# Kernel tuning notes

Measured on AMD Instinct MI355X. Metric: run time of the kernel, lower is better.

Reference implementation:

```python
import jax, jax.numpy as jnp
import numpy as np

G, NPG, C, H, F, L = 256, 128, 16, 128, 128, 3
N = G * NPG          # 32768 nodes
E = 524288           # 16 edges per node on average
REG, REG_C = 0.01, 0.01
LN_EPS = 1e-5


def setup_inputs() -> dict:
    key = jax.random.key(0)
    ks = jax.random.split(key, 20)
    x = jax.random.normal(ks[0], (N, F), dtype=jnp.float32)
    # edges kept within each graph so dense pooling matches to_dense_batch semantics
    epg = E // G
    offs = jnp.repeat(jnp.arange(G, dtype=jnp.int64) * NPG, epg)
    src = jax.random.randint(ks[1], (E,), 0, NPG, dtype=jnp.int64) + offs
    tgt = jax.random.randint(ks[2], (E,), 0, NPG, dtype=jnp.int64) + offs
    edge_index = jnp.stack([src, tgt])
    mask_breaks = jax.random.bernoulli(ks[3], 0.5, (E,))
    s = jax.random.uniform(ks[4], (N, C), dtype=jnp.float32)
    batch = jnp.repeat(jnp.arange(G, dtype=jnp.int64), NPG)
    sc = 1.0 / np.sqrt(H)
    Wn = jax.random.normal(ks[5], (L, H, H), dtype=jnp.float32) * sc
    bn_ = jax.random.normal(ks[6], (L, H), dtype=jnp.float32) * sc
    Wo = jax.random.normal(ks[7], (L, H, H), dtype=jnp.float32) * sc
    bo = jax.random.normal(ks[8], (L, H), dtype=jnp.float32) * sc
    Wr = jax.random.normal(ks[9], (L, H, H), dtype=jnp.float32) * sc
    ln_g = jnp.ones((L, H), dtype=jnp.float32)
    ln_b = jnp.zeros((L, H), dtype=jnp.float32)
    fln_g = jnp.ones((H,), dtype=jnp.float32)
    fln_b = jnp.zeros((H,), dtype=jnp.float32)
    lin_w = jax.random.normal(ks[10], (1, H), dtype=jnp.float32) * sc
    bias = jnp.zeros((1,), dtype=jnp.float32)
    return {"x": x, "edge_index": edge_index, "mask_breaks": mask_breaks, "s": s,
            "batch": batch, "Wn": Wn, "bn_": bn_, "Wo": Wo, "bo": bo, "Wr": Wr,
            "ln_g": ln_g, "ln_b": ln_b, "fln_g": fln_g, "fln_b": fln_b,
            "lin_w": lin_w, "bias": bias}


def _layernorm(h, g, b):
    mu = jnp.mean(h, axis=-1, keepdims=True)
    v = jnp.mean(jnp.square(h - mu), axis=-1, keepdims=True)
    return (h - mu) * jax.lax.rsqrt(v + LN_EPS) * g + b


def reference(x, edge_index, mask_breaks, s, batch, Wn, bn_, Wo, bo, Wr,
              ln_g, ln_b, fln_g, fln_b, lin_w, bias):
    src, tgt = edge_index[0], edge_index[1]
    ones_e = jnp.ones((E,), dtype=x.dtype)
    cnt = jax.ops.segment_sum(ones_e, tgt, num_segments=N)          # in-degree
    inv_cnt = (1.0 / jnp.maximum(cnt, 1.0))[:, None]
    h = x
    for i in range(L):
        x_in = h @ Wn[i].T + bn_[i]
        x_out = h @ Wo[i].T + bo[i]
        x_root = h @ Wr[i].T
        msg = jnp.where(mask_breaks[:, None], x_in[src], x_out[src])  # [E,H]
        agg = jax.ops.segment_sum(msg, tgt, num_segments=N) * inv_cnt  # mean aggr
        h = jax.nn.relu(_layernorm(agg + x_root, ln_g[i], ln_b[i]))
    # dense per-graph views (equal-size graphs, batch ids sorted -> reshape)
    xd = h.reshape(G, NPG, H)
    sd = s.reshape(G, NPG, C)
    pooled = jnp.einsum("gnc,gnh->gch", sd, xd)                      # [G,C,H]
    pooled = _layernorm(pooled, fln_g, fln_b)
    xc = pooled @ lin_w.T                                            # [G,C,1]
    col_sum = sd.sum(axis=1)                                          # [G,C]
    cmask = (col_sum > 0)[..., None]
    xc = xc * cmask.astype(xc.dtype)
    out = xc.sum(axis=1) + bias                                      # [G,1]
    reg_loss = jnp.abs(Wo).sum() + jnp.abs(bo).sum()
    denom = (cmask.astype(xc.dtype).squeeze(-1) + 1e-7).sum(axis=1, keepdims=True)
    l1_loss = (jnp.abs(xc).sum(axis=1) / denom).mean()
    losses = REG * reg_loss + REG_C * l1_loss
    return out, losses, xc
```

## Files before the change

### kernel.cpp

```cpp
#include <hip/hip_runtime.h>

#define NN   32768
#define HD   128
#define EE   524288
#define GG   256
#define EPG  2048
#define CCd  16
#define LLd  3

typedef short short8 __attribute__((ext_vector_type(8)));
typedef float f32x4 __attribute__((ext_vector_type(4)));

__device__ __forceinline__ unsigned short f2bf(float f) {
  unsigned u = __builtin_bit_cast(unsigned, f);
  return (unsigned short)((u + 0x7FFFu + ((u >> 16) & 1u)) >> 16);
}
__device__ __forceinline__ unsigned bfpack(float a, float b) {
  return (unsigned)f2bf(a) | ((unsigned)f2bf(b) << 16);
}

__global__ __launch_bounds__(256) void convert_w_kernel(const float* __restrict__ Wn, const float* __restrict__ Wo,
                                                        const float* __restrict__ Wr, const float* __restrict__ bo,
                                                        unsigned* __restrict__ Wnb, unsigned* __restrict__ Wob,
                                                        unsigned* __restrict__ Wrb, float* __restrict__ wsreg) {
  int i = blockIdx.x * 256 + threadIdx.x;
  float4 a = *(const float4*)(Wn + (size_t)i * 4);
  float4 b = *(const float4*)(Wo + (size_t)i * 4);
  float4 c = *(const float4*)(Wr + (size_t)i * 4);
  *(uint2*)(Wnb + (size_t)i * 2) = make_uint2(bfpack(a.x, a.y), bfpack(a.z, a.w));
  *(uint2*)(Wob + (size_t)i * 2) = make_uint2(bfpack(b.x, b.y), bfpack(b.z, b.w));
  *(uint2*)(Wrb + (size_t)i * 2) = make_uint2(bfpack(c.x, c.y), bfpack(c.z, c.w));
  float s = fabsf(b.x) + fabsf(b.y) + fabsf(b.z) + fabsf(b.w);
  if (blockIdx.x == 0 && threadIdx.x < 96) {
    float4 d = *(const float4*)(bo + threadIdx.x * 4);
    s += fabsf(d.x) + fabsf(d.y) + fabsf(d.z) + fabsf(d.w);
  }
#pragma unroll
  for (int mk = 1; mk < 64; mk <<= 1) s += __shfl_xor(s, mk, 64);
  if ((threadIdx.x & 63) == 0) atomicAdd(wsreg, s);
}

__global__ __launch_bounds__(256) void build_m_kernel(const int* __restrict__ src, const int* __restrict__ tgt,
                                                      const int* __restrict__ mask,
                                                      unsigned* __restrict__ Mb, float* __restrict__ fin,
                                                      float* __restrict__ fout) {
  __shared__ unsigned Mi[2 * 128 * 64];
  const int g = blockIdx.x;
  const int tid = threadIdx.x;
  for (int i = tid; i < 16384; i += 256) Mi[i] = 0;
  __syncthreads();
  const int e0 = g * EPG;
#pragma unroll
  for (int i = 0; i < 8; ++i) {
    int e = e0 + i * 256 + tid;
    int t = tgt[e] & 127;
    int sl = src[e] & 127;
    int dir = (mask[e] != 0) ? 0 : 1;
    atomicAdd(&Mi[dir * 8192 + t * 64 + (sl >> 1)], 1u << ((sl & 1) * 16));
  }
  __syncthreads();
  const int t = tid >> 1, p = tid & 1;
  unsigned nin = 0, nout = 0;
#pragma unroll 4
  for (int k = 0; k < 32; ++k) { unsigned v = Mi[t * 64 + p * 32 + k]; nin += (v & 0xffffu) + (v >> 16); }
#pragma unroll 4
  for (int k = 0; k < 32; ++k) { unsigned v = Mi[8192 + t * 64 + p * 32 + k]; nout += (v & 0xffffu) + (v >> 16); }
  nin += __shfl_xor((int)nin, 1);
  nout += __shfl_xor((int)nout, 1);
  unsigned dg = nin + nout;
  float inv = 1.0f / (float)(dg > 0 ? dg : 1);
  if (p == 0) { fin[g * 128 + t] = (float)nin * inv; fout[g * 128 + t] = (float)nout * inv; }
#pragma unroll
  for (int dir = 0; dir < 2; ++dir) {
    int base = dir * 8192 + t * 64 + p * 32;
#pragma unroll
    for (int k4 = 0; k4 < 8; ++k4) {
      uint4 v = *(const uint4*)&Mi[base + k4 * 4];
      uint4 o;
      o.x = bfpack((float)(v.x & 0xffffu) * inv, (float)(v.x >> 16) * inv);
      o.y = bfpack((float)(v.y & 0xffffu) * inv, (float)(v.y >> 16) * inv);
      o.z = bfpack((float)(v.z & 0xffffu) * inv, (float)(v.z >> 16) * inv);
      o.w = bfpack((float)(v.w & 0xffffu) * inv, (float)(v.w >> 16) * inv);
      *(uint4*)&Mb[(size_t)g * 16384 + base + k4 * 4] = o;
    }
  }
}

struct PF { uint4 a, b; };
__device__ __forceinline__ PF pf_load(const unsigned short* __restrict__ srcb, int tid) {
  int row = tid >> 2, c = tid & 3;
  const unsigned short* p = srcb + row * 128 + c * 8;
  PF r;
  r.a = *(const uint4*)p;
  r.b = *(const uint4*)(p + 32);
  return r;
}
__device__ __forceinline__ void pf_store(unsigned short* __restrict__ buf, const PF& r, int tid) {
  int row = tid >> 2, c = tid & 3;
  *(uint4*)(buf + row * 72 + c * 8) = r.a;
  *(uint4*)(buf + row * 72 + (c + 4) * 8) = r.b;
}
__device__ __forceinline__ const unsigned short* stage_ptr(int sIdx, const unsigned short* Mg,
                                                           const unsigned short* Wnb, const unsigned short* Wob,
                                                           const unsigned short* Wrb) {
  if (sIdx > 29) sIdx = 29;
  int L = sIdx / 10;
  int r = sIdx - L * 10;
  int half = r & 1;
  int op = r >> 1;
  const unsigned short* base;
  if (op == 0) base = Mg;
  else if (op == 1) base = Wnb + L * 16384;
  else if (op == 2) base = Mg + 16384;
  else if (op == 3) base = Wob + L * 16384;
  else base = Wrb + L * 16384;
  return base + half * 64;
}

__global__ __launch_bounds__(512) void fused_kernel(
    const float* __restrict__ x, const unsigned short* __restrict__ Mb,
    const unsigned short* __restrict__ Wnb, const unsigned short* __restrict__ Wob,
    const unsigned short* __restrict__ Wrb,
    const float* __restrict__ bn, const float* __restrict__ bo,
    const float* __restrict__ fin, const float* __restrict__ fout,
    const float* __restrict__ lng, const float* __restrict__ lnb,
    const float* __restrict__ s,
    const float* __restrict__ flng, const float* __restrict__ flnb,
    const float* __restrict__ linw, const float* __restrict__ bias,
    float* __restrict__ out, float* __restrict__ l1g) {
  __shared__ unsigned short hTs[128 * 136];
  __shared__ unsigned short sTs[16 * 136];
  __shared__ unsigned short buf[128 * 72];
  __shared__ float colsumS[CCd];
  __shared__ float xcs[CCd], axcs[CCd], msk[CCd];

  const int g = blockIdx.x;
  const int tid = threadIdx.x;
  const int wave = tid >> 6;
  const int lane = tid & 63;
  const int m = lane & 15;
  const int q = lane >> 4;
  const int t0 = wave << 4;
  const unsigned short* Mg = Mb + (size_t)g * 32768;

  int sIdx = 0;
  PF pf = pf_load(stage_ptr(0, Mg, Wnb, Wob, Wrb), tid);

  {
    const float4* xg = (const float4*)(x + (size_t)g * 16384);
#pragma unroll
    for (int i = 0; i < 8; ++i) {
      int flat = i * 512 + tid;
      int t = flat >> 5, f0 = (flat & 31) << 2;
      float4 v = xg[flat];
      hTs[(f0 + 0) * 136 + t] = f2bf(v.x);
      hTs[(f0 + 1) * 136 + t] = f2bf(v.y);
      hTs[(f0 + 2) * 136 + t] = f2bf(v.z);
      hTs[(f0 + 3) * 136 + t] = f2bf(v.w);
    }
    int t = tid >> 2, c0 = (tid & 3) << 2;
    float4 v = *(const float4*)(s + (size_t)g * 2048 + t * 16 + c0);
    sTs[(c0 + 0) * 136 + t] = f2bf(v.x);
    sTs[(c0 + 1) * 136 + t] = f2bf(v.y);
    sTs[(c0 + 2) * 136 + t] = f2bf(v.z);
    sTs[(c0 + 3) * 136 + t] = f2bf(v.w);
    if (tid < CCd) {
      float cs = 0.f;
      for (int tt = 0; tt < 128; ++tt) cs += s[(size_t)g * 2048 + tt * 16 + tid];
      colsumS[tid] = cs;
    }
  }

  for (int L = 0; L < LLd; ++L) {
    f32x4 pre[8];
#pragma unroll
    for (int ct = 0; ct < 8; ++ct) pre[ct] = (f32x4){0.f, 0.f, 0.f, 0.f};

    for (int sg = 0; sg < 2; ++sg) {
      f32x4 accT[8];
#pragma unroll
      for (int ft = 0; ft < 8; ++ft) accT[ft] = (f32x4){0.f, 0.f, 0.f, 0.f};
#pragma unroll
      for (int half = 0; half < 2; ++half) {
        __syncthreads();
        pf_store(buf, pf, tid);
        ++sIdx;
        pf = pf_load(stage_ptr(sIdx, Mg, Wnb, Wob, Wrb), tid);
        __syncthreads();
#pragma unroll
        for (int ksl = 0; ksl < 2; ++ksl) {
          const int ksg = half * 2 + ksl;
          short8 bfr = *(const short8*)&buf[(t0 + m) * 72 + ksl * 32 + q * 8];
#pragma unroll
          for (int ft = 0; ft < 8; ++ft) {
            short8 afr = *(const short8*)&hTs[(ft * 16 + m) * 136 + ksg * 32 + q * 8];
            accT[ft] = __builtin_amdgcn_mfma_f32_16x16x32_bf16(afr, bfr, accT[ft], 0, 0, 0);
          }
        }
      }
#pragma unroll
      for (int half = 0; half < 2; ++half) {
        __syncthreads();
        pf_store(buf, pf, tid);
        ++sIdx;
        pf = pf_load(stage_ptr(sIdx, Mg, Wnb, Wob, Wrb), tid);
        __syncthreads();
#pragma unroll
        for (int ksl = 0; ksl < 2; ++ksl) {
          const int ksg = half * 2 + ksl;
          f32x4 lo = accT[2 * ksg], hi = accT[2 * ksg + 1];
          short8 afr;
#pragma unroll
          for (int j = 0; j < 8; ++j) {
            int srcl = ((((q & 1) << 1) + (j >> 2)) << 4) + m;
            float ylo = __shfl(lo[j & 3], srcl, 64);
            float yhi = __shfl(hi[j & 3], srcl, 64);
            afr[j] = (short)f2bf((q >> 1) ? yhi : ylo);
          }
#pragma unroll
          for (int ct = 0; ct < 8; ++ct) {
            short8 bfr = *(const short8*)&buf[(ct * 16 + m) * 72 + ksl * 32 + q * 8];
            pre[ct] = __builtin_amdgcn_mfma_f32_16x16x32_bf16(afr, bfr, pre[ct], 0, 0, 0);
          }
        }
      }
    }
#pragma unroll
    for (int half = 0; half < 2; ++half) {
      __syncthreads();
      pf_store(buf, pf, tid);
      ++sIdx;
      pf = pf_load(stage_ptr(sIdx, Mg, Wnb, Wob, Wrb), tid);
      __syncthreads();
#pragma unroll
      for (int ksl = 0; ksl < 2; ++ksl) {
        const int ksg = half * 2 + ksl;
        short8 afr;
#pragma unroll
        for (int j = 0; j < 8; ++j)
          afr[j] = (short)hTs[(ksg * 32 + q * 8 + j) * 136 + t0 + m];
#pragma unroll
        for (int ct = 0; ct < 8; ++ct) {
          short8 bfr = *(const short8*)&buf[(ct * 16 + m) * 72 + ksl * 32 + q * 8];
          pre[ct] = __builtin_amdgcn_mfma_f32_16x16x32_bf16(afr, bfr, pre[ct], 0, 0, 0);
        }
      }
    }
    float bnv[8], bov[8], gv[8], bv[8];
#pragma unroll
    for (int ct = 0; ct < 8; ++ct) {
      int c = L * 128 + ct * 16 + m;
      bnv[ct] = bn[c]; bov[ct] = bo[c]; gv[ct] = lng[c]; bv[ct] = lnb[c];
    }
#pragma unroll
    for (int r = 0; r < 4; ++r) {
      const int tl = q * 4 + r;
      const int T = g * 128 + t0 + tl;
      const float fiv = fin[T], fov = fout[T];
      float v[8];
      float sum = 0.f;
#pragma unroll
      for (int ct = 0; ct < 8; ++ct) {
        v[ct] = pre[ct][r] + fiv * bnv[ct] + fov * bov[ct];
        sum += v[ct];
      }
      sum += __shfl_xor(sum, 1); sum += __shfl_xor(sum, 2);
      sum += __shfl_xor(sum, 4); sum += __shfl_xor(sum, 8);
      const float mu = sum * (1.0f / 128.0f);
      float sq = 0.f;
#pragma unroll
      for (int ct = 0; ct < 8; ++ct) { float d = v[ct] - mu; sq += d * d; }
      sq += __shfl_xor(sq, 1); sq += __shfl_xor(sq, 2);
      sq += __shfl_xor(sq, 4); sq += __shfl_xor(sq, 8);
      const float rstd = rsqrtf(sq * (1.0f / 128.0f) + 1e-5f);
#pragma unroll
      for (int ct = 0; ct < 8; ++ct) {
        float o = fmaxf((v[ct] - mu) * rstd * gv[ct] + bv[ct], 0.0f);
        hTs[(ct * 16 + m) * 136 + t0 + tl] = f2bf(o);
      }
    }
  }

  __syncthreads();
  f32x4 pl = (f32x4){0.f, 0.f, 0.f, 0.f};
#pragma unroll
  for (int ks = 0; ks < 4; ++ks) {
    short8 a = *(const short8*)&sTs[m * 136 + ks * 32 + q * 8];
    short8 b = *(const short8*)&hTs[(wave * 16 + m) * 136 + ks * 32 + q * 8];
    pl = __builtin_amdgcn_mfma_f32_16x16x32_bf16(a, b, pl, 0, 0, 0);
  }
  float* pooledS = (float*)buf;
#pragma unroll
  for (int r = 0; r < 4; ++r) pooledS[(q * 4 + r) * 132 + wave * 16 + m] = pl[r];
  __syncthreads();

  if (tid < 256) {
    const int c = tid >> 4;
    const int j0 = (tid & 15) << 3;
    float v[8];
#pragma unroll
    for (int jj = 0; jj < 8; ++jj) v[jj] = pooledS[c * 132 + j0 + jj];
    float sum = 0.f;
#pragma unroll
    for (int jj = 0; jj < 8; ++jj) sum += v[jj];
#pragma unroll
    for (int mk = 1; mk < 16; mk <<= 1) sum += __shfl_xor(sum, mk, 64);
    float mu = sum * (1.0f / 128.0f);
    float sq = 0.f;
#pragma unroll
    for (int jj = 0; jj < 8; ++jj) { float d = v[jj] - mu; sq += d * d; }
#pragma unroll
    for (int mk = 1; mk < 16; mk <<= 1) sq += __shfl_xor(sq, mk, 64);
    float rstd = rsqrtf(sq * (1.0f / 128.0f) + 1e-5f);
    float dot = 0.f;
#pragma unroll
    for (int jj = 0; jj < 8; ++jj) {
      float nv = (v[jj] - mu) * rstd * flng[j0 + jj] + flnb[j0 + jj];
      dot += nv * linw[j0 + jj];
    }
#pragma unroll
    for (int mk = 1; mk < 16; mk <<= 1) dot += __shfl_xor(dot, mk, 64);
    if ((tid & 15) == 0) {
      float cm = (colsumS[c] > 0.f) ? 1.0f : 0.0f;
      float xcv = dot * cm;
      out[257 + g * CCd + c] = xcv;
      xcs[c] = xcv; axcs[c] = fabsf(xcv); msk[c] = cm;
    }
  }
  __syncthreads();
  if (tid == 0) {
    float so = 0.f, sa = 0.f, sd = 0.f;
#pragma unroll
    for (int k = 0; k < CCd; ++k) { so += xcs[k]; sa += axcs[k]; sd += msk[k] + 1e-7f; }
    out[g] = so + bias[0];
    l1g[g] = sa / sd;
  }
}

__global__ __launch_bounds__(256) void combine_kernel(const float* __restrict__ l1g, const float* __restrict__ wsreg,
                                                      float* __restrict__ outp) {
  const int tid = threadIdx.x;
  float s2 = l1g[tid];
#pragma unroll
  for (int mk = 1; mk < 64; mk <<= 1) s2 += __shfl_xor(s2, mk, 64);
  __shared__ float rs2[4];
  if ((tid & 63) == 0) rs2[tid >> 6] = s2;
  __syncthreads();
  if (tid == 0) {
    float l1 = (rs2[0] + rs2[1] + rs2[2] + rs2[3]) * (1.0f / GG);
    outp[0] = 0.01f * wsreg[0] + 0.01f * l1;
  }
}

extern "C" void kernel_launch(void* const* d_in, const int* in_sizes, int n_in,
                              void* d_out, int out_size, void* d_ws, size_t ws_size,
                              hipStream_t stream) {
  (void)in_sizes; (void)n_in; (void)out_size; (void)ws_size;
  const float* x    = (const float*)d_in[0];
  const int*   ei   = (const int*)d_in[1];
  const int*   mask = (const int*)d_in[2];
  const float* s    = (const float*)d_in[3];
  const float* Wn   = (const float*)d_in[5];
  const float* bn   = (const float*)d_in[6];
  const float* Wo   = (const float*)d_in[7];
  const float* bo   = (const float*)d_in[8];
  const float* Wr   = (const float*)d_in[9];
  const float* lng  = (const float*)d_in[10];
  const float* lnb  = (const float*)d_in[11];
  const float* flng = (const float*)d_in[12];
  const float* flnb = (const float*)d_in[13];
  const float* linw = (const float*)d_in[14];
  const float* bias = (const float*)d_in[15];
  float* out = (float*)d_out;

  char* ws = (char*)d_ws;
  size_t off = 0;
  auto alloc = [&](size_t b) { char* p = ws + off; off += (b + 255) & ~(size_t)255; return p; };
  unsigned short* Mbuf = (unsigned short*)alloc((size_t)GG * 2 * 128 * 128 * 2);
  float* fin    = (float*)alloc((size_t)NN * 4);
  float* fout   = (float*)alloc((size_t)NN * 4);
  unsigned short* Wnb = (unsigned short*)alloc((size_t)LLd * HD * HD * 2);
  unsigned short* Wob = (unsigned short*)alloc((size_t)LLd * HD * HD * 2);
  unsigned short* Wrb = (unsigned short*)alloc((size_t)LLd * HD * HD * 2);
  float* l1g    = (float*)alloc((size_t)GG * 4);
  float* wsreg  = (float*)alloc(256);

  const int* srcA = ei;
  const int* tgtA = ei + EE;

  hipMemsetAsync(wsreg, 0, 4, stream);
  convert_w_kernel<<<LLd * HD * HD / (256 * 4), 256, 0, stream>>>(Wn, Wo, Wr, bo,
      (unsigned*)Wnb, (unsigned*)Wob, (unsigned*)Wrb, wsreg);
  build_m_kernel<<<GG, 256, 0, stream>>>(srcA, tgtA, mask, (unsigned*)Mbuf, fin, fout);
  fused_kernel<<<GG, 512, 0, stream>>>(x, Mbuf, Wnb, Wob, Wrb, bn, bo, fin, fout,
                                       lng, lnb, s, flng, flnb, linw, bias, out, l1g);
  combine_kernel<<<1, 256, 0, stream>>>(l1g, wsreg, out + 256);
}
```

Before: 157.3 us.

## Fuse adjacency build into main kernel and keep adjacency fragments in registers

Removes the separate build_m kernel and its global bf16 adjacency buffer. Each block now builds per-graph edge counts in shared memory, computes degrees and normalized bf16 MFMA fragments directly into registers, and stores fin/fout in shared memory. The staged shared-memory prefetch of weights is replaced by direct global (L2-cached) loads of the bf16 weight fragments, which removes many syncthreads. The x transpose is also rewritten to pack pairs of nodes per store. The costs are higher register pressure from holding the fragments plus a launch-bounds hint, and weight reads that now go through cache rather than shared memory.

```diff
diff --git a/kernel.cpp b/kernel.cpp
--- a/kernel.cpp
+++ b/kernel.cpp
@@ -40,99 +40,22 @@
   if ((threadIdx.x & 63) == 0) atomicAdd(wsreg, s);
 }
 
-__global__ __launch_bounds__(256) void build_m_kernel(const int* __restrict__ src, const int* __restrict__ tgt,
-                                                      const int* __restrict__ mask,
-                                                      unsigned* __restrict__ Mb, float* __restrict__ fin,
-                                                      float* __restrict__ fout) {
-  __shared__ unsigned Mi[2 * 128 * 64];
-  const int g = blockIdx.x;
-  const int tid = threadIdx.x;
-  for (int i = tid; i < 16384; i += 256) Mi[i] = 0;
-  __syncthreads();
-  const int e0 = g * EPG;
-#pragma unroll
-  for (int i = 0; i < 8; ++i) {
-    int e = e0 + i * 256 + tid;
-    int t = tgt[e] & 127;
-    int sl = src[e] & 127;
-    int dir = (mask[e] != 0) ? 0 : 1;
-    atomicAdd(&Mi[dir * 8192 + t * 64 + (sl >> 1)], 1u << ((sl & 1) * 16));
-  }
-  __syncthreads();
-  const int t = tid >> 1, p = tid & 1;
-  unsigned nin = 0, nout = 0;
-#pragma unroll 4
-  for (int k = 0; k < 32; ++k) { unsigned v = Mi[t * 64 + p * 32 + k]; nin += (v & 0xffffu) + (v >> 16); }
-#pragma unroll 4
-  for (int k = 0; k < 32; ++k) { unsigned v = Mi[8192 + t * 64 + p * 32 + k]; nout += (v & 0xffffu) + (v >> 16); }
-  nin += __shfl_xor((int)nin, 1);
-  nout += __shfl_xor((int)nout, 1);
-  unsigned dg = nin + nout;
-  float inv = 1.0f / (float)(dg > 0 ? dg : 1);
-  if (p == 0) { fin[g * 128 + t] = (float)nin * inv; fout[g * 128 + t] = (float)nout * inv; }
-#pragma unroll
-  for (int dir = 0; dir < 2; ++dir) {
-    int base = dir * 8192 + t * 64 + p * 32;
-#pragma unroll
-    for (int k4 = 0; k4 < 8; ++k4) {
-      uint4 v = *(const uint4*)&Mi[base + k4 * 4];
-      uint4 o;
-      o.x = bfpack((float)(v.x & 0xffffu) * inv, (float)(v.x >> 16) * inv);
-      o.y = bfpack((float)(v.y & 0xffffu) * inv, (float)(v.y >> 16) * inv);
-      o.z = bfpack((float)(v.z & 0xffffu) * inv, (float)(v.z >> 16) * inv);
-      o.w = bfpack((float)(v.w & 0xffffu) * inv, (float)(v.w >> 16) * inv);
-      *(uint4*)&Mb[(size_t)g * 16384 + base + k4 * 4] = o;
-    }
-  }
-}
-
-struct PF { uint4 a, b; };
-__device__ __forceinline__ PF pf_load(const unsigned short* __restrict__ srcb, int tid) {
-  int row = tid >> 2, c = tid & 3;
-  const unsigned short* p = srcb + row * 128 + c * 8;
-  PF r;
-  r.a = *(const uint4*)p;
-  r.b = *(const uint4*)(p + 32);
-  return r;
-}
-__device__ __forceinline__ void pf_store(unsigned short* __restrict__ buf, const PF& r, int tid) {
-  int row = tid >> 2, c = tid & 3;
-  *(uint4*)(buf + row * 72 + c * 8) = r.a;
-  *(uint4*)(buf + row * 72 + (c + 4) * 8) = r.b;
-}
-__device__ __forceinline__ const unsigned short* stage_ptr(int sIdx, const unsigned short* Mg,
-                                                           const unsigned short* Wnb, const unsigned short* Wob,
-                                                           const unsigned short* Wrb) {
-  if (sIdx > 29) sIdx = 29;
-  int L = sIdx / 10;
-  int r = sIdx - L * 10;
-  int half = r & 1;
-  int op = r >> 1;
-  const unsigned short* base;
-  if (op == 0) base = Mg;
-  else if (op == 1) base = Wnb + L * 16384;
-  else if (op == 2) base = Mg + 16384;
-  else if (op == 3) base = Wob + L * 16384;
-  else base = Wrb + L * 16384;
-  return base + half * 64;
-}
-
-__global__ __launch_bounds__(512) void fused_kernel(
-    const float* __restrict__ x, const unsigned short* __restrict__ Mb,
+__global__ __launch_bounds__(512, 2) void fused_kernel(
+    const float* __restrict__ x,
+    const int* __restrict__ esrc, const int* __restrict__ etgt, const int* __restrict__ emask,
     const unsigned short* __restrict__ Wnb, const unsigned short* __restrict__ Wob,
     const unsigned short* __restrict__ Wrb,
     const float* __restrict__ bn, const float* __restrict__ bo,
-    const float* __restrict__ fin, const float* __restrict__ fout,
     const float* __restrict__ lng, const float* __restrict__ lnb,
     const float* __restrict__ s,
     const float* __restrict__ flng, const float* __restrict__ flnb,
     const float* __restrict__ linw, const float* __restrict__ bias,
     float* __restrict__ out, float* __restrict__ l1g) {
-  __shared__ unsigned short hTs[128 * 136];
-  __shared__ unsigned short sTs[16 * 136];
-  __shared__ unsigned short buf[128 * 72];
-  __shared__ float colsumS[CCd];
-  __shared__ float xcs[CCd], axcs[CCd], msk[CCd];
+  __shared__ __align__(16) unsigned short hTs[128 * 136];
+  __shared__ __align__(16) unsigned short sTs[16 * 136];
+  __shared__ __align__(16) unsigned cnt[2 * 128 * 64];
+  __shared__ float finS[128], foutS[128];
+  __shared__ float colsumS[CCd], xcs[CCd], axcs[CCd], msk[CCd];
 
   const int g = blockIdx.x;
   const int tid = threadIdx.x;
@@ -141,34 +64,97 @@
   const int m = lane & 15;
   const int q = lane >> 4;
   const int t0 = wave << 4;
-  const unsigned short* Mg = Mb + (size_t)g * 32768;
-
-  int sIdx = 0;
-  PF pf = pf_load(stage_ptr(0, Mg, Wnb, Wob, Wrb), tid);
 
   {
-    const float4* xg = (const float4*)(x + (size_t)g * 16384);
-#pragma unroll
-    for (int i = 0; i < 8; ++i) {
-      int flat = i * 512 + tid;
-      int t = flat >> 5, f0 = (flat & 31) << 2;
-      float4 v = xg[flat];
-      hTs[(f0 + 0) * 136 + t] = f2bf(v.x);
-      hTs[(f0 + 1) * 136 + t] = f2bf(v.y);
-      hTs[(f0 + 2) * 136 + t] = f2bf(v.z);
-      hTs[(f0 + 3) * 136 + t] = f2bf(v.w);
-    }
-    int t = tid >> 2, c0 = (tid & 3) << 2;
-    float4 v = *(const float4*)(s + (size_t)g * 2048 + t * 16 + c0);
-    sTs[(c0 + 0) * 136 + t] = f2bf(v.x);
-    sTs[(c0 + 1) * 136 + t] = f2bf(v.y);
-    sTs[(c0 + 2) * 136 + t] = f2bf(v.z);
-    sTs[(c0 + 3) * 136 + t] = f2bf(v.w);
-    if (tid < CCd) {
+    uint4* cz = (uint4*)cnt;
+#pragma unroll
+    for (int i = 0; i < 8; ++i) cz[i * 512 + tid] = make_uint4(0u, 0u, 0u, 0u);
+
+    const float* xg = x + (size_t)g * 16384;
+    unsigned* hw = (unsigned*)hTs;
+#pragma unroll
+    for (int i = 0; i < 4; ++i) {
+      int task = i * 512 + tid;
+      int t2 = task & 63;
+      int f0 = (task >> 6) << 2;
+      float4 va = *(const float4*)(xg + (2 * t2) * 128 + f0);
+      float4 vb = *(const float4*)(xg + (2 * t2 + 1) * 128 + f0);
+      hw[(f0 + 0) * 68 + t2] = bfpack(va.x, vb.x);
+      hw[(f0 + 1) * 68 + t2] = bfpack(va.y, vb.y);
+      hw[(f0 + 2) * 68 + t2] = bfpack(va.z, vb.z);
+      hw[(f0 + 3) * 68 + t2] = bfpack(va.w, vb.w);
+    }
+    {
+      int t = tid >> 2, c0 = (tid & 3) << 2;
+      float4 v = *(const float4*)(s + (size_t)g * 2048 + t * 16 + c0);
+      sTs[(c0 + 0) * 136 + t] = f2bf(v.x);
+      sTs[(c0 + 1) * 136 + t] = f2bf(v.y);
+      sTs[(c0 + 2) * 136 + t] = f2bf(v.z);
+      sTs[(c0 + 3) * 136 + t] = f2bf(v.w);
+    }
+    if (tid < 64) {
+      int c = tid & 15, qq = tid >> 4;
       float cs = 0.f;
-      for (int tt = 0; tt < 128; ++tt) cs += s[(size_t)g * 2048 + tt * 16 + tid];
-      colsumS[tid] = cs;
-    }
+      for (int tt = qq; tt < 128; tt += 4) cs += s[(size_t)g * 2048 + tt * 16 + c];
+      cs += __shfl_xor(cs, 16); cs += __shfl_xor(cs, 32);
+      if (qq == 0) colsumS[c] = cs;
+    }
+  }
+  __syncthreads();
+
+  {
+    const int e0 = g * EPG;
+#pragma unroll
+    for (int i = 0; i < 4; ++i) {
+      int e = e0 + i * 512 + tid;
+      int t = etgt[e] & 127;
+      int sl = esrc[e] & 127;
+      int dir = (emask[e] != 0) ? 0 : 1;
+      atomicAdd(&cnt[dir * 8192 + t * 64 + (sl >> 1)], 1u << ((sl & 1) * 16));
+    }
+  }
+  __syncthreads();
+
+  short8 mfr[2][2][2];
+  {
+    const int t = t0 + m;
+    unsigned nin = 0, nout = 0;
+    uint4 cw[2][2][2];
+#pragma unroll
+    for (int d = 0; d < 2; ++d)
+#pragma unroll
+      for (int hf = 0; hf < 2; ++hf)
+#pragma unroll
+        for (int ksl = 0; ksl < 2; ++ksl) {
+          uint4 v = *(const uint4*)&cnt[d * 8192 + t * 64 + hf * 32 + ksl * 16 + q * 4];
+          cw[d][hf][ksl] = v;
+          unsigned ssum = (v.x & 0xffffu) + (v.x >> 16) + (v.y & 0xffffu) + (v.y >> 16)
+                        + (v.z & 0xffffu) + (v.z >> 16) + (v.w & 0xffffu) + (v.w >> 16);
+          if (d == 0) nin += ssum; else nout += ssum;
+        }
+    nin += __shfl_xor((int)nin, 16);  nin += __shfl_xor((int)nin, 32);
+    nout += __shfl_xor((int)nout, 16); nout += __shfl_xor((int)nout, 32);
+    unsigned dg = nin + nout;
+    float inv = 1.0f / (float)(dg > 0 ? dg : 1);
+    if (q == 0) { finS[t] = (float)nin * inv; foutS[t] = (float)nout * inv; }
+#pragma unroll
+    for (int d = 0; d < 2; ++d)
+#pragma unroll
+      for (int hf = 0; hf < 2; ++hf)
+#pragma unroll
+        for (int ksl = 0; ksl < 2; ++ksl) {
+          uint4 v = cw[d][hf][ksl];
+          short8 f;
+          f[0] = (short)f2bf((float)(v.x & 0xffffu) * inv);
+          f[1] = (short)f2bf((float)(v.x >> 16) * inv);
+          f[2] = (short)f2bf((float)(v.y & 0xffffu) * inv);
+          f[3] = (short)f2bf((float)(v.y >> 16) * inv);
+          f[4] = (short)f2bf((float)(v.z & 0xffffu) * inv);
+          f[5] = (short)f2bf((float)(v.z >> 16) * inv);
+          f[6] = (short)f2bf((float)(v.w & 0xffffu) * inv);
+          f[7] = (short)f2bf((float)(v.w >> 16) * inv);
+          mfr[d][hf][ksl] = f;
+        }
   }
 
   for (int L = 0; L < LLd; ++L) {
@@ -176,38 +162,29 @@
 #pragma unroll
     for (int ct = 0; ct < 8; ++ct) pre[ct] = (f32x4){0.f, 0.f, 0.f, 0.f};
 
+#pragma unroll
     for (int sg = 0; sg < 2; ++sg) {
+      const unsigned short* Wg = (sg == 0 ? Wnb : Wob) + L * 16384;
       f32x4 accT[8];
 #pragma unroll
       for (int ft = 0; ft < 8; ++ft) accT[ft] = (f32x4){0.f, 0.f, 0.f, 0.f};
 #pragma unroll
-      for (int half = 0; half < 2; ++half) {
-        __syncthreads();
-        pf_store(buf, pf, tid);
-        ++sIdx;
-        pf = pf_load(stage_ptr(sIdx, Mg, Wnb, Wob, Wrb), tid);
-        __syncthreads();
-#pragma unroll
-        for (int ksl = 0; ksl < 2; ++ksl) {
-          const int ksg = half * 2 + ksl;
-          short8 bfr = *(const short8*)&buf[(t0 + m) * 72 + ksl * 32 + q * 8];
+      for (int hf = 0; hf < 2; ++hf)
+#pragma unroll
+        for (int ksl = 0; ksl < 2; ++ksl) {
+          const int ksg = hf * 2 + ksl;
+          short8 bfr = mfr[sg][hf][ksl];
 #pragma unroll
           for (int ft = 0; ft < 8; ++ft) {
             short8 afr = *(const short8*)&hTs[(ft * 16 + m) * 136 + ksg * 32 + q * 8];
             accT[ft] = __builtin_amdgcn_mfma_f32_16x16x32_bf16(afr, bfr, accT[ft], 0, 0, 0);
           }
         }
-      }
-#pragma unroll
-      for (int half = 0; half < 2; ++half) {
-        __syncthreads();
-        pf_store(buf, pf, tid);
-        ++sIdx;
-        pf = pf_load(stage_ptr(sIdx, Mg, Wnb, Wob, Wrb), tid);
-        __syncthreads();
-#pragma unroll
-        for (int ksl = 0; ksl < 2; ++ksl) {
-          const int ksg = half * 2 + ksl;
+#pragma unroll
+      for (int hf = 0; hf < 2; ++hf)
+#pragma unroll
+        for (int ksl = 0; ksl < 2; ++ksl) {
+          const int ksg = hf * 2 + ksl;
           f32x4 lo = accT[2 * ksg], hi = accT[2 * ksg + 1];
           short8 afr;
 #pragma unroll
@@ -219,69 +196,67 @@
           }
 #pragma unroll
           for (int ct = 0; ct < 8; ++ct) {
-            short8 bfr = *(const short8*)&buf[(ct * 16 + m) * 72 + ksl * 32 + q * 8];
+            short8 bfr = *(const short8*)&Wg[(ct * 16 + m) * 128 + ksg * 32 + q * 8];
             pre[ct] = __builtin_amdgcn_mfma_f32_16x16x32_bf16(afr, bfr, pre[ct], 0, 0, 0);
           }
         }
+    }
+    {
+      const unsigned short* Wrg = Wrb + L * 16384;
+#pragma unroll
+      for (int hf = 0; hf < 2; ++hf)
+#pragma unroll
+        for (int ksl = 0; ksl < 2; ++ksl) {
+          const int ksg = hf * 2 + ksl;
+          short8 afr;
+#pragma unroll
+          for (int j = 0; j < 8; ++j)
+            afr[j] = (short)hTs[(ksg * 32 + q * 8 + j) * 136 + t0 + m];
+#pragma unroll
+          for (int ct = 0; ct < 8; ++ct) {
+            short8 bfr = *(const short8*)&Wrg[(ct * 16 + m) * 128 + ksg * 32 + q * 8];
+            pre[ct] = __builtin_amdgcn_mfma_f32_16x16x32_bf16(afr, bfr, pre[ct], 0, 0, 0);
+          }
+        }
+    }
+    __syncthreads();
+    {
+      float bnv[8], bov[8], gv[8], bv[8];
+#pragma unroll
+      for (int ct = 0; ct < 8; ++ct) {
+        int c = L * 128 + ct * 16 + m;
+        bnv[ct] = bn[c]; bov[ct] = bo[c]; gv[ct] = lng[c]; bv[ct] = lnb[c];
       }
-    }
-#pragma unroll
-    for (int half = 0; half < 2; ++half) {
-      __syncthreads();
-      pf_store(buf, pf, tid);
-      ++sIdx;
-      pf = pf_load(stage_ptr(sIdx, Mg, Wnb, Wob, Wrb), tid);
-      __syncthreads();
-#pragma unroll
-      for (int ksl = 0; ksl < 2; ++ksl) {
-        const int ksg = half * 2 + ksl;
-        short8 afr;
-#pragma unroll
-        for (int j = 0; j < 8; ++j)
-          afr[j] = (short)hTs[(ksg * 32 + q * 8 + j) * 136 + t0 + m];
+#pragma unroll
+      for (int r = 0; r < 4; ++r) {
+        const int tl = q * 4 + r;
+        const float fiv = finS[t0 + tl], fov = foutS[t0 + tl];
+        float v[8];
+        float sum = 0.f;
 #pragma unroll
         for (int ct = 0; ct < 8; ++ct) {
-          short8 bfr = *(const short8*)&buf[(ct * 16 + m) * 72 + ksl * 32 + q * 8];
-          pre[ct] = __builtin_amdgcn_mfma_f32_16x16x32_bf16(afr, bfr, pre[ct], 0, 0, 0);
+          v[ct] = pre[ct][r] + fiv * bnv[ct] + fov * bov[ct];
+          sum += v[ct];
+        }
+        sum += __shfl_xor(sum, 1); sum += __shfl_xor(sum, 2);
+        sum += __shfl_xor(sum, 4); sum += __shfl_xor(sum, 8);
+        const float mu = sum * (1.0f / 128.0f);
+        float sq = 0.f;
+#pragma unroll
+        for (int ct = 0; ct < 8; ++ct) { float d = v[ct] - mu; sq += d * d; }
+        sq += __shfl_xor(sq, 1); sq += __shfl_xor(sq, 2);
+        sq += __shfl_xor(sq, 4); sq += __shfl_xor(sq, 8);
+        const float rstd = rsqrtf(sq * (1.0f / 128.0f) + 1e-5f);
+#pragma unroll
+        for (int ct = 0; ct < 8; ++ct) {
+          float o = fmaxf((v[ct] - mu) * rstd * gv[ct] + bv[ct], 0.0f);
+          hTs[(ct * 16 + m) * 136 + t0 + tl] = f2bf(o);
         }
       }
     }
-    float bnv[8], bov[8], gv[8], bv[8];
-#pragma unroll
-    for (int ct = 0; ct < 8; ++ct) {
-      int c = L * 128 + ct * 16 + m;
-      bnv[ct] = bn[c]; bov[ct] = bo[c]; gv[ct] = lng[c]; bv[ct] = lnb[c];
-    }
-#pragma unroll
-    for (int r = 0; r < 4; ++r) {
-      const int tl = q * 4 + r;
-      const int T = g * 128 + t0 + tl;
-      const float fiv = fin[T], fov = fout[T];
-      float v[8];
-      float sum = 0.f;
-#pragma unroll
-      for (int ct = 0; ct < 8; ++ct) {
-        v[ct] = pre[ct][r] + fiv * bnv[ct] + fov * bov[ct];
-        sum += v[ct];
-      }
-      sum += __shfl_xor(sum, 1); sum += __shfl_xor(sum, 2);
-      sum += __shfl_xor(sum, 4); sum += __shfl_xor(sum, 8);
-      const float mu = sum * (1.0f / 128.0f);
-      float sq = 0.f;
-#pragma unroll
-      for (int ct = 0; ct < 8; ++ct) { float d = v[ct] - mu; sq += d * d; }
-      sq += __shfl_xor(sq, 1); sq += __shfl_xor(sq, 2);
-      sq += __shfl_xor(sq, 4); sq += __shfl_xor(sq, 8);
-      const float rstd = rsqrtf(sq * (1.0f / 128.0f) + 1e-5f);
-#pragma unroll
-      for (int ct = 0; ct < 8; ++ct) {
-        float o = fmaxf((v[ct] - mu) * rstd * gv[ct] + bv[ct], 0.0f);
-        hTs[(ct * 16 + m) * 136 + t0 + tl] = f2bf(o);
-      }
-    }
-  }
-
-  __syncthreads();
+    __syncthreads();
+  }
+
   f32x4 pl = (f32x4){0.f, 0.f, 0.f, 0.f};
 #pragma unroll
   for (int ks = 0; ks < 4; ++ks) {
@@ -289,7 +264,7 @@
     short8 b = *(const short8*)&hTs[(wave * 16 + m) * 136 + ks * 32 + q * 8];
     pl = __builtin_amdgcn_mfma_f32_16x16x32_bf16(a, b, pl, 0, 0, 0);
   }
-  float* pooledS = (float*)buf;
+  float* pooledS = (float*)cnt;
 #pragma unroll
   for (int r = 0; r < 4; ++r) pooledS[(q * 4 + r) * 132 + wave * 16 + m] = pl[r];
   __syncthreads();
@@ -376,9 +351,6 @@
   char* ws = (char*)d_ws;
   size_t off = 0;
   auto alloc = [&](size_t b) { char* p = ws + off; off += (b + 255) & ~(size_t)255; return p; };
-  unsigned short* Mbuf = (unsigned short*)alloc((size_t)GG * 2 * 128 * 128 * 2);
-  float* fin    = (float*)alloc((size_t)NN * 4);
-  float* fout   = (float*)alloc((size_t)NN * 4);
   unsigned short* Wnb = (unsigned short*)alloc((size_t)LLd * HD * HD * 2);
   unsigned short* Wob = (unsigned short*)alloc((size_t)LLd * HD * HD * 2);
   unsigned short* Wrb = (unsigned short*)alloc((size_t)LLd * HD * HD * 2);
@@ -391,8 +363,7 @@
   hipMemsetAsync(wsreg, 0, 4, stream);
   convert_w_kernel<<<LLd * HD * HD / (256 * 4), 256, 0, stream>>>(Wn, Wo, Wr, bo,
       (unsigned*)Wnb, (unsigned*)Wob, (unsigned*)Wrb, wsreg);
-  build_m_kernel<<<GG, 256, 0, stream>>>(srcA, tgtA, mask, (unsigned*)Mbuf, fin, fout);
-  fused_kernel<<<GG, 512, 0, stream>>>(x, Mbuf, Wnb, Wob, Wrb, bn, bo, fin, fout,
+  fused_kernel<<<GG, 512, 0, stream>>>(x, srcA, tgtA, mask, Wnb, Wob, Wrb, bn, bo,
                                        lng, lnb, s, flng, flnb, linw, bias, out, l1g);
   combine_kernel<<<1, 256, 0, stream>>>(l1g, wsreg, out + 256);
 }
```

After: 251.8 us. 1.6x slower.
